# Kernel tuning notes

Hardware: AMD Instinct MI355X
Metric: run time of the kernel (lower is better)

The kernel has to match this reference:

```python
import jax, jax.numpy as jnp
import numpy as np

N = 1024  # batch


def setup_inputs() -> dict:
    key = jax.random.key(0)
    ks = jax.random.split(key, 10)
    meta_feature = jax.random.uniform(ks[0], (N, 6), dtype=jnp.float32)
    tile_wall_feature = jax.random.uniform(ks[1], (N, 34, 5), dtype=jnp.float32)
    tile_prep = jax.random.uniform(ks[2], (N, 320, 34, 7), dtype=jnp.float32)
    # keep tile_hidden_ct (channel 4) away from 0 so the division stays well-conditioned
    tile_prep = tile_prep.at[..., 4].add(0.5)
    fan_prep = jax.random.uniform(ks[3], (N, 320, 80), dtype=jnp.float32)
    redundant_tile_prep = jax.random.uniform(ks[4], (N, 320, 34), dtype=jnp.float32)
    count_prep = jax.random.uniform(ks[5], (N, 320), dtype=jnp.float32)
    chi_peng_count_remain = jax.random.uniform(ks[6], (N, 320), dtype=jnp.float32)
    # learned params: Linear(11,1) of TileProbModuleNew, fan_coeff, tile_coeff
    W_throw = jax.random.normal(ks[7], (11,), dtype=jnp.float32) * 0.05
    b_throw = jnp.array(0.5, dtype=jnp.float32)  # keeps prob_throw > 0 (faithful math; avoids NaN from neg**frac)
    fan_coeff = 0.1 + 0.015 * jax.random.normal(ks[8], (80,), dtype=jnp.float32)
    tile_coeff = 1.0 + 0.015 * jax.random.normal(ks[9], (34,), dtype=jnp.float32)
    fan_coeff_multiplier = jnp.ones((80,), dtype=jnp.float32).at[33].set(21.0)
    return {
        'meta_feature': meta_feature,
        'tile_wall_feature': tile_wall_feature,
        'tile_prep': tile_prep,
        'fan_prep': fan_prep,
        'redundant_tile_prep': redundant_tile_prep,
        'count_prep': count_prep,
        'chi_peng_count_remain': chi_peng_count_remain,
        'W_throw': W_throw,
        'b_throw': b_throw,
        'fan_coeff': fan_coeff,
        'fan_coeff_multiplier': fan_coeff_multiplier,
        'tile_coeff': tile_coeff,
    }


def reference(meta_feature, tile_wall_feature, tile_prep, fan_prep,
              redundant_tile_prep, count_prep, chi_peng_count_remain,
              W_throw, b_throw, fan_coeff, fan_coeff_multiplier, tile_coeff):
    n = meta_feature.shape[0]
    # TileProbModuleNew: per-tile Linear(11,1)
    meta_exp = jnp.broadcast_to(meta_feature[:, None, :], (n, 34, 6))
    feat = jnp.concatenate([meta_exp, tile_wall_feature], axis=-1)        # (n,34,11)
    prob_throw = feat @ W_throw + b_throw                                  # (n,34)

    tile_self_draw_baseline = tile_prep[..., 0]
    tile_need_count = tile_prep[..., 1]
    tile_cp_coeff = tile_prep[..., 2]
    tile_cp_base = tile_prep[..., 3]
    tile_hidden_ct = tile_prep[..., 4]
    tile_cp_switch = tile_prep[..., 5]
    tile_null_filler = tile_prep[..., 6]

    fan_pref = fan_prep * fan_coeff * fan_coeff_multiplier                 # (n,320,80)
    multiplied_fan_pref = jnp.sum(fan_pref, axis=-1)                       # (n,320)

    term1 = tile_self_draw_baseline * prob_throw[:, None, :] ** tile_need_count
    term2 = jnp.nan_to_num(tile_cp_base * tile_cp_coeff / tile_hidden_ct)
    terms_summed = term1 + tile_null_filler + term2 * tile_cp_switch      # (n,320,34)

    final_prob_throw = jnp.prod(terms_summed, axis=-1) * 100.0 * multiplied_fan_pref  # (n,320)

    redundant_prob = redundant_tile_prep * final_prob_throw[..., None]    # (n,320,34)
    redundant_prob = redundant_prob.reshape(n, 5, 64, 34)
    tile_bound_winrate = redundant_prob.sum(axis=2)                        # (n,5,34)

    weighted_tile_prob = (tile_bound_winrate * tile_coeff)[:, 0]           # (n,34)

    final_prob_ops = final_prob_throw.reshape(n, 5, 64).sum(axis=-1)       # (n,5)
    max_tile_prob_for_action = jnp.max(tile_bound_winrate, axis=2)         # (n,5)
    max_tile_prob_for_action = max_tile_prob_for_action.at[:, 0].set(final_prob_ops[:, 0])
    return (max_tile_prob_for_action, weighted_tile_prob)
```

## Files before the change

kernel.cpp:

```cpp
#include <hip/hip_runtime.h>
#include <math.h>

#define N_OPS 320

__global__ __launch_bounds__(256) void mahjong_kernel(
    const float* __restrict__ meta,
    const float* __restrict__ wall,
    const float* __restrict__ tile_prep,
    const float* __restrict__ fan_prep,
    const float* __restrict__ redundant,
    const float* __restrict__ W_throw,
    const float* __restrict__ b_throw,
    const float* __restrict__ fan_coeff,
    const float* __restrict__ fan_mult,
    const float* __restrict__ tile_coeff,
    float* __restrict__ out_max,
    float* __restrict__ out_weighted,
    int n)
{
    const int blk  = blockIdx.x;
    const int b    = blk / 5;
    const int g    = blk % 5;
    const int tid  = threadIdx.x;
    const int wave = tid >> 6;
    const int lane = tid & 63;

    __shared__ float terms_sm[32 * 34];
    __shared__ float qp_sm[32 * 21];
    __shared__ float prob_sm[34];
    __shared__ float fc_sm[80];
    __shared__ float final_sm[32];
    __shared__ float acc_sm[4][34];

    if (tid < 34) {
        float acc = b_throw[0];
        #pragma unroll
        for (int j = 0; j < 6; ++j) acc += meta[(size_t)b * 6 + j] * W_throw[j];
        const float* w = wall + ((size_t)b * 34 + tid) * 5;
        #pragma unroll
        for (int j = 0; j < 5; ++j) acc += w[j] * W_throw[6 + j];
        prob_sm[tid] = acc;
    }
    if (tid >= 64 && tid < 144) {
        int f = tid - 64;
        fc_sm[f] = fan_coeff[f] * fan_mult[f];
    }
    __syncthreads();

    float acc3 = 0.0f;
    float fsum_part = 0.0f;

    const int t_init = tid % 34;

    for (int c = 0; c < 2; ++c) {
        const size_t row0 = (size_t)b * N_OPS + g * 64 + c * 32;

        if (c) __syncthreads();

        {
            const float* tp0 = tile_prep + row0 * 238;
            int t = t_init;
            #pragma unroll
            for (int k = 0; k < 4; ++k) {
                const int tau = tid + 256 * k;
                const float* e = tp0 + 7 * tau;
                float c0 = e[0], c1 = e[1], c2 = e[2], c3 = e[3];
                float c4 = e[4], c5 = e[5], c6 = e[6];
                float term = c0 * exp2f(c1 * log2f(prob_sm[t])) + c6 + (c3 * c2 / c4) * c5;
                terms_sm[tau] = term;
                t += 18; if (t >= 34) t -= 34;
            }
            if (tid < 64) {
                const int tau = 1024 + tid;
                int t2 = tid + 4;
                if (t2 >= 34) t2 -= 34;
                if (t2 >= 34) t2 -= 34;
                const float* e = tp0 + 7 * tau;
                float c0 = e[0], c1 = e[1], c2 = e[2], c3 = e[3];
                float c4 = e[4], c5 = e[5], c6 = e[6];
                float term = c0 * exp2f(c1 * log2f(prob_sm[t2])) + c6 + (c3 * c2 / c4) * c5;
                terms_sm[tau] = term;
            }
        }

        {
            const float4* fsrc = (const float4*)(fan_prep + row0 * 80);
            #pragma unroll
            for (int k = 0; k < 3; ++k) {
                const int i = tid + 256 * k;
                if (i < 640) {
                    float4 v = fsrc[i];
                    const int r = i / 20;
                    const int q = i - r * 20;
                    const int f = 4 * q;
                    qp_sm[r * 21 + q] = v.x * fc_sm[f]     + v.y * fc_sm[f + 1]
                                      + v.z * fc_sm[f + 2] + v.w * fc_sm[f + 3];
                }
            }
        }
        __syncthreads();

        if (tid < 32) {
            const float* tr = terms_sm + tid * 34;
            float p = 1.0f;
            #pragma unroll
            for (int t = 0; t < 34; ++t) p *= tr[t];
            const float* qr = qp_sm + tid * 21;
            float q = 0.0f;
            #pragma unroll
            for (int j = 0; j < 20; ++j) q += qr[j];
            float fin = p * 100.0f * q;
            final_sm[tid] = fin;
            fsum_part += fin;
        }
        __syncthreads();

        if (lane < 34) {
            const float* rr0 = redundant + (row0 + wave * 8) * 34;
            #pragma unroll
            for (int i = 0; i < 8; ++i)
                acc3 += rr0[i * 34 + lane] * final_sm[wave * 8 + i];
        }
    }

    if (lane < 34) acc_sm[wave][lane] = acc3;
    __syncthreads();

    if (wave == 0) {
        float tbw = 0.0f;
        if (lane < 34)
            tbw = acc_sm[0][lane] + acc_sm[1][lane] + acc_sm[2][lane] + acc_sm[3][lane];
        if (g == 0) {
            if (lane < 34)
                out_weighted[(size_t)b * 34 + lane] = tbw * tile_coeff[lane];
            float fs = fsum_part;
            #pragma unroll
            for (int sh = 1; sh < 64; sh <<= 1) fs += __shfl_xor(fs, sh);
            if (lane == 0) out_max[(size_t)b * 5] = fs;
        } else {
            float m = (lane < 34) ? tbw : -INFINITY;
            #pragma unroll
            for (int sh = 1; sh < 64; sh <<= 1) m = fmaxf(m, __shfl_xor(m, sh));
            if (lane == 0) out_max[(size_t)b * 5 + g] = m;
        }
    }
}

extern "C" void kernel_launch(void* const* d_in, const int* in_sizes, int n_in,
                              void* d_out, int out_size, void* d_ws, size_t ws_size,
                              hipStream_t stream) {
    const float* meta       = (const float*)d_in[0];
    const float* wall       = (const float*)d_in[1];
    const float* tile_prep  = (const float*)d_in[2];
    const float* fan_prep   = (const float*)d_in[3];
    const float* redundant  = (const float*)d_in[4];
    const float* W_throw    = (const float*)d_in[7];
    const float* b_throw    = (const float*)d_in[8];
    const float* fan_coeff  = (const float*)d_in[9];
    const float* fan_mult   = (const float*)d_in[10];
    const float* tile_coeff = (const float*)d_in[11];

    int n = in_sizes[0] / 6;
    float* out_max      = (float*)d_out;
    float* out_weighted = out_max + (size_t)n * 5;

    dim3 grid(n * 5), block(256);
    hipLaunchKernelGGL(mahjong_kernel, grid, block, 0, stream,
                       meta, wall, tile_prep, fan_prep, redundant,
                       W_throw, b_throw, fan_coeff, fan_mult, tile_coeff,
                       out_max, out_weighted, n);
}
```

Baseline: 512.2 us.

## Stage tile_prep through LDS with float4 loads in smaller row chunks

The kernel now copies tile_prep rows into shared memory with coalesced float4 loads and computes the per-tile terms from LDS, replacing the stride-7 scalar global reads. To fit the staging buffer, each chunk shrinks from 32 to 16 rows, giving four chunks per block instead of two. The aim is better global-memory coalescing on the dominant input stream. The cost is an extra barrier per chunk, more chunk iterations, and larger LDS use that may lower occupancy.

```diff
diff --git a/kernel.cpp b/kernel.cpp
--- a/kernel.cpp
+++ b/kernel.cpp
@@ -2,6 +2,10 @@
 #include <math.h>
 
 #define N_OPS 320
+#define CROWS 16
+#define TPF (CROWS * 238)
+#define TPV (TPF / 4)
+#define FANV (CROWS * 20)
 
 __global__ __launch_bounds__(256) void mahjong_kernel(
     const float* __restrict__ meta,
@@ -25,11 +29,12 @@
     const int wave = tid >> 6;
     const int lane = tid & 63;
 
-    __shared__ float terms_sm[32 * 34];
-    __shared__ float qp_sm[32 * 21];
+    __shared__ __align__(16) float tp_sm[TPF];
+    __shared__ float terms_sm[CROWS * 34];
+    __shared__ float qp_sm[CROWS * 21];
     __shared__ float prob_sm[34];
     __shared__ float fc_sm[80];
-    __shared__ float final_sm[32];
+    __shared__ float final_sm[CROWS];
     __shared__ float acc_sm[4][34];
 
     if (tid < 34) {
@@ -50,45 +55,24 @@
     float acc3 = 0.0f;
     float fsum_part = 0.0f;
 
-    const int t_init = tid % 34;
-
-    for (int c = 0; c < 2; ++c) {
-        const size_t row0 = (size_t)b * N_OPS + g * 64 + c * 32;
+    for (int c = 0; c < 4; ++c) {
+        const size_t row0 = (size_t)b * N_OPS + g * 64 + c * CROWS;
 
         if (c) __syncthreads();
 
         {
-            const float* tp0 = tile_prep + row0 * 238;
-            int t = t_init;
+            const float4* tsrc = (const float4*)(tile_prep + row0 * 238);
+            float4* tdst = (float4*)tp_sm;
             #pragma unroll
             for (int k = 0; k < 4; ++k) {
-                const int tau = tid + 256 * k;
-                const float* e = tp0 + 7 * tau;
-                float c0 = e[0], c1 = e[1], c2 = e[2], c3 = e[3];
-                float c4 = e[4], c5 = e[5], c6 = e[6];
-                float term = c0 * exp2f(c1 * log2f(prob_sm[t])) + c6 + (c3 * c2 / c4) * c5;
-                terms_sm[tau] = term;
-                t += 18; if (t >= 34) t -= 34;
+                const int i = tid + 256 * k;
+                if (i < TPV) tdst[i] = tsrc[i];
             }
-            if (tid < 64) {
-                const int tau = 1024 + tid;
-                int t2 = tid + 4;
-                if (t2 >= 34) t2 -= 34;
-                if (t2 >= 34) t2 -= 34;
-                const float* e = tp0 + 7 * tau;
-                float c0 = e[0], c1 = e[1], c2 = e[2], c3 = e[3];
-                float c4 = e[4], c5 = e[5], c6 = e[6];
-                float term = c0 * exp2f(c1 * log2f(prob_sm[t2])) + c6 + (c3 * c2 / c4) * c5;
-                terms_sm[tau] = term;
-            }
-        }
-
-        {
             const float4* fsrc = (const float4*)(fan_prep + row0 * 80);
             #pragma unroll
-            for (int k = 0; k < 3; ++k) {
+            for (int k = 0; k < 2; ++k) {
                 const int i = tid + 256 * k;
-                if (i < 640) {
+                if (i < FANV) {
                     float4 v = fsrc[i];
                     const int r = i / 20;
                     const int q = i - r * 20;
@@ -100,7 +84,22 @@
         }
         __syncthreads();
 
-        if (tid < 32) {
+        #pragma unroll
+        for (int k = 0; k < 3; ++k) {
+            const int tau = tid + 256 * k;
+            if (tau < CROWS * 34) {
+                const int r = tau / 34;
+                const int t = tau - r * 34;
+                const float* e = tp_sm + 7 * tau;
+                float c0 = e[0], c1 = e[1], c2 = e[2], c3 = e[3];
+                float c4 = e[4], c5 = e[5], c6 = e[6];
+                terms_sm[tau] = c0 * exp2f(c1 * log2f(prob_sm[t])) + c6
+                              + (c3 * c2 / c4) * c5;
+            }
+        }
+        __syncthreads();
+
+        if (tid < CROWS) {
             const float* tr = terms_sm + tid * 34;
             float p = 1.0f;
             #pragma unroll
@@ -116,10 +115,10 @@
         __syncthreads();
 
         if (lane < 34) {
-            const float* rr0 = redundant + (row0 + wave * 8) * 34;
+            const float* rr0 = redundant + (row0 + wave * 4) * 34;
             #pragma unroll
-            for (int i = 0; i < 8; ++i)
-                acc3 += rr0[i * 34 + lane] * final_sm[wave * 8 + i];
+            for (int i = 0; i < 4; ++i)
+                acc3 += rr0[i * 34 + lane] * final_sm[wave * 4 + i];
         }
     }
 
```

Result: slower. 525.0 us (+2.5%).
